# Optimization experiments

Measured on AMD Instinct MI355X. Metric: run time of the kernel, lower is better.

The kernel has to match this reference:

```python
import jax, jax.numpy as jnp
import numpy as np

R = 2                                   # NMS radius (init kwarg r)
EPS = float(np.finfo(np.float32).eps)   # torch.finfo(float32).eps
PI = float(np.pi)


def _sobel(x):
    """Kornia SpatialGradient (sobel, normalized): x [N,1,H,W] -> (dx, dy) each [N,1,H,W]."""
    kx = jnp.array([[-1., 0., 1.], [-2., 0., 2.], [-1., 0., 1.]], jnp.float32) / 8.0
    ky = kx.T
    k = jnp.stack([kx, ky])[:, None]    # [2,1,3,3] -> out channels dx, dy
    xp = jnp.pad(x, ((0, 0), (0, 0), (1, 1), (1, 1)), mode='edge')  # replicate pad
    out = jax.lax.conv_general_dilated(xp, k, (1, 1), 'VALID',
                                       dimension_numbers=('NCHW', 'OIHW', 'NCHW'))
    return out[:, 0:1], out[:, 1:2]


def _theta(mask):
    """Edge direction from one-hot mask, per STEAL edges_nms. mask [N,1,H,W]."""
    dx, dy = _sobel(mask)
    gxx, _ = _sobel(dx)
    gxy, gyy = _sobel(dy)
    return jnp.fmod(jnp.arctan(gyy * jnp.sign(-gxy + EPS) / (gxx + EPS)), PI)


def setup_inputs() -> dict:
    key = jax.random.key(0)
    k1, k2 = jax.random.split(key)
    pred_labels = jax.random.normal(k1, (4, 16, 512, 1024), dtype=jnp.float32)
    true_labels = jax.random.randint(k2, (4, 512, 1024), 0, 16, dtype=jnp.int64)
    return {"pred_labels": pred_labels, "true_labels": true_labels}


def reference(pred_labels, true_labels):
    B, C, H, W = pred_labels.shape
    # per-class one-hot masks -> direction maps
    onehot = jax.nn.one_hot(true_labels, C, dtype=jnp.float32)        # [B,H,W,C]
    masks = onehot.transpose(0, 3, 1, 2).reshape(B * C, 1, H, W)
    theta = _theta(masks).reshape(B, C, H, W)
    thresh_theta = jnp.fmod(jnp.round(theta * (5.0 / PI)) + 5.0, 5.0)  # {0..4}
    dirs = jnp.fmod(thresh_theta, 4.0).astype(jnp.int32)               # {0,1,2,3}

    exp_p = jnp.exp(pred_labels)
    js = list(range(-R, R))
    # offsets (dx_off, dy_off) summed in the denominator for each direction
    offs = {
        0: [(0, j) for j in js],        # horizontal: preds[x, y-r:y+r]
        1: [(j, -j - 1) for j in js],   # anti-diagonal
        2: [(j, 0) for j in js],        # vertical: preds[x-r:x+r, y]
        3: [(-j - 1, j) for j in js],   # anti-diagonal (reversed traversal, same set)
    }
    denom = jnp.ones_like(exp_p)
    for d in range(4):
        dd = exp_p * 0.0
        for ox, oy in offs[d]:
            dd = dd + jnp.roll(exp_p, (-ox, -oy), axis=(2, 3))  # exp_p[x+ox, y+oy]
        denom = jnp.where(dirs == d, dd, denom)

    interior = jnp.zeros((H, W), bool).at[R:H - R, R:W - R].set(True)
    nms = jnp.where(interior, exp_p / denom, 0.0)
    return jnp.sum(nms)
```

## Files before the change

kernel.cpp:

```cpp
#include <hip/hip_runtime.h>


#define Bn 4
#define Cn 16
#define Hn 512
#define Wn 1024

typedef unsigned long long u64;
typedef unsigned int u32;
typedef float f4u __attribute__((ext_vector_type(4), aligned(4)));
typedef int   i4u __attribute__((ext_vector_type(4), aligned(4)));

static __device__ __forceinline__ float fast_rcp(float x) {
#if __has_builtin(__builtin_amdgcn_rcpf)
  return __builtin_amdgcn_rcpf(x);
#else
  return 1.0f / x;
#endif
}


#define P1TW 128
#define P1TH 8
#define P1LW 132
#define P1LH 12

__global__ __launch_bounds__(256)
void dir_kernel(const int* __restrict__ labels, u32* __restrict__ dirs)
{
  __shared__ unsigned char labt[P1LH][P1LW];

  const int w0 = blockIdx.x * P1TW;
  const int h0 = blockIdx.y * P1TH;
  const int b  = blockIdx.z;
  const int tid = threadIdx.x;

  const int* lbase = labels + (size_t)b * (Hn*Wn);
  const bool interior = (h0 >= 2) && (h0 + P1TH + 2 <= Hn) &&
                        (w0 >= 2) && (w0 + P1TW + 2 <= Wn);
  if (interior) {
    const int* lb = lbase + (size_t)(h0-2)*Wn + (w0-2);
    for (int i = tid; i < P1LH*33; i += 256) {
      int row = i / 33, c4 = (i - row*33) * 4;
      i4u L = *(const i4u*)(lb + row*Wn + c4);
      *(u32*)&labt[row][c4] =
          (u32)L.x | ((u32)L.y << 8) | ((u32)L.z << 16) | ((u32)L.w << 24);
    }
  } else {
    for (int i = tid; i < P1LH*33; i += 256) {
      int row = i / 33, c4 = (i - row*33) * 4;
      int gh = min(max(h0-2+row, 0), Hn-1);
      const int* lr = lbase + gh*Wn;
      u32 v = 0;
      #pragma unroll
      for (int k = 0; k < 4; ++k) {
        int gw = min(max(w0-2+c4+k, 0), Wn-1);
        v |= (u32)(lr[gw] & 0xff) << (8*k);
      }
      *(u32*)&labt[row][c4] = v;
    }
  }
  __syncthreads();

  const int tcol = tid & 31;
  const int trow = tid >> 5;

  u64 W[5];
  #pragma unroll
  for (int r = 0; r < 5; ++r) {
    const u32* lp = (const u32*)&labt[trow + r][0];
    u64 lo = lp[tcol];
    u64 hi = lp[tcol + 1];
    W[r] = lo | (hi << 32);
  }

  u32 pack[4] = {0u, 0u, 0u, 0u};

  #pragma unroll 1
  for (int c = 0; c < 16; ++c) {
    const u64 crep = 0x0101010101010101ULL * (u32)c;
    u64 m[5];
    #pragma unroll
    for (int r = 0; r < 5; ++r) {
      u64 x = W[r] ^ crep;
      m[r] = ((0x8080808080808080ULL - x) & 0x8080808080808080ULL) >> 7;
    }
    u64 t  = m[1] + m[3];
    u64 VA = m[0] + m[4] + (t << 2) + (m[2] << 2) + (m[2] << 1);
    u64 VB = ((m[3] << 1) + m[4] + 0x0303030303030303ULL)
             - (m[0] + (m[1] << 1));
    u64 VC = (m[0] + m[4] + 0x0202020202020202ULL) - (m[2] << 1);
    u64 gxxp = (VA + (VA >> 32) + 0x4040404040404040ULL) - ((VA >> 16) << 1);
    u64 q1   = (VC >> 8) + (VC >> 24);
    u64 w16  = VC >> 16;
    u64 gyyp = (VC + (VC >> 32)) + (q1 << 2) + (w16 << 2) + (w16 << 1);
    u64 gxyp = (((VB >> 24) << 1) + (VB >> 32) + 0x2020202020202020ULL)
             - (VB + ((VB >> 8) << 1));

    u32 gxxl = (u32)gxxp, gyyl = (u32)gyyp, gxyl = (u32)gxyp;
    #pragma unroll
    for (int k = 0; k < 4; ++k) {
      int gxx = (int)((gxxl >> (8*k)) & 0xffu) - 64;
      int gyy = (int)((gyyl >> (8*k)) & 0xffu) - 32;
      int gxyb = (int)((gxyl >> (8*k)) & 0xffu);
      int ax = gxx < 0 ? -gxx : gxx;
      int ay = gyy < 0 ? -gyy : gyy;
      int t1 = (__mul24(ay, 100)  > __mul24(ax, 33))   ? 1 : 0;
      int t2 = (__mul24(ay, 1000) > __mul24(ax, 1377)) ? 1 : 0;
      int rb = t1 + t2;
      bool ng = ((gyy < 0) != (gxyb > 32)) != (gxx < 0);
      int dir = ng ? ((rb == 2) ? 3 : 0) : rb;
      pack[k] |= (u32)dir << (2*c);
    }
  }

  const int gh = h0 + trow;
  u32* drow = dirs + ((size_t)b*Hn + gh)*Wn + (w0 + 4*tcol);
  *(uint4*)drow = make_uint4(pack[0], pack[1], pack[2], pack[3]);
}


#define TW 128
#define TH 32
#define LW 132
#define LH 36
#define NT 256

__global__ __launch_bounds__(NT)
void nms_sum_kernel(const float* __restrict__ pred,
                    const u32* __restrict__ dirs,
                    float* __restrict__ slots)
{
  __shared__ float ext[LH*LW];
  __shared__ float wsum[NT/64];

  const int w0 = blockIdx.x * TW;
  const int h0 = blockIdx.y * TH;
  const int bz = blockIdx.z;
  const int b  = bz >> 4;
  const int c  = bz & 15;
  const int tid = threadIdx.x;

  const int x  = tid & 127;
  const int rg = tid >> 7;
  const int gw = w0 + x;

  const u32* dbase = dirs + (size_t)b*Hn*Wn + (size_t)(h0 + rg*16)*Wn + gw;
  u32 dv[16];
  #pragma unroll
  for (int r = 0; r < 16; ++r) dv[r] = dbase[(size_t)r*Wn];

  const float* plane = pred + (size_t)(b*Cn + c) * (size_t)(Hn*Wn);
  const bool interior = (h0 >= 2) && (h0 + TH + 2 <= Hn) &&
                        (w0 >= 2) && (w0 + TW + 2 <= Wn);
  if (interior) {
    const float* pb = plane + (size_t)(h0-2)*Wn + (w0-2);
    for (int i = tid; i < LH*33; i += NT) {
      int row = i / 33, c4 = (i - row*33) * 4;
      f4u p = *(const f4u*)(pb + row*Wn + c4);
      float4 e;
      e.x = __expf(p.x); e.y = __expf(p.y); e.z = __expf(p.z); e.w = __expf(p.w);
      *(float4*)&ext[row*LW + c4] = e;
    }
  } else {
    for (int i = tid; i < LH*(LW/2); i += NT) {
      int row = i / (LW/2);
      int col = (i - row*(LW/2)) * 2;
      int gh = min(max(h0-2+row, 0), Hn-1);
      int ga = min(max(w0-2+col,   0), Wn-1);
      int gb = min(max(w0-1+col,   0), Wn-1);
      const float* prow = plane + gh*Wn;
      *(float2*)&ext[row*LW+col] = make_float2(__expf(prow[ga]), __expf(prow[gb]));
    }
  }
  __syncthreads();

  const bool wv = (gw >= 2) && (gw < Wn-2);
  const u32 sh = 2u * (u32)c;
  const int ghb = h0 + rg*16;

  float acc = 0.f;
  const int abase = (rg*16 + 2)*LW + (x + 2);

  #pragma unroll
  for (int r = 0; r < 16; ++r) {
    const int a0 = abase + r*LW;
    const int dir = (int)((dv[r] >> sh) & 3u);

    const int o0 = (dir == 0) ? -2 : ((dir == 2) ? -264 : -263);
    const int o1 = (dir == 0) ? -1 : -132;
    const int o2 = -(dir & 1);
    const int o3 = (dir == 0) ?  1 : ((dir == 2) ?  132 :  130);

    float g0 = ext[a0 + o0];
    float g1 = ext[a0 + o1];
    float g2 = ext[a0 + o2];
    float g3 = ext[a0 + o3];
    float num = ext[a0];
    float den = ((g0 + g1) + g2) + g3;

    const int gh = ghb + r;
    const bool hv = (gh >= 2) && (gh < Hn-2);
    float nn = (hv && wv) ? num : 0.f;
    acc += nn * fast_rcp(den);
  }

  const int lane = tid & 63;
  const int wq   = tid >> 6;
  #pragma unroll
  for (int off = 32; off > 0; off >>= 1)
    acc += __shfl_down(acc, off);
  if (lane == 0) wsum[wq] = acc;
  __syncthreads();
  if (tid == 0) {
    float s = 0.f;
    #pragma unroll
    for (int q = 0; q < NT/64; ++q) s += wsum[q];
    atomicAdd(&slots[(bz << 2) | (blockIdx.x & 3)], s);
  }
}

__global__ __launch_bounds__(64)
void reduce_ws_kernel(const float* __restrict__ slots, float* __restrict__ out)
{
  const int l = threadIdx.x;
  float s = (slots[l] + slots[l + 64]) + (slots[l + 128] + slots[l + 192]);
  #pragma unroll
  for (int off = 32; off > 0; off >>= 1)
    s += __shfl_down(s, off);
  if (l == 0) *out = s;
}

extern "C" void kernel_launch(void* const* d_in, const int* in_sizes, int n_in,
                              void* d_out, int out_size, void* d_ws, size_t ws_size,
                              hipStream_t stream) {
  (void)in_sizes; (void)n_in; (void)ws_size; (void)out_size;
  const float* pred   = (const float*)d_in[0];
  const int*   labels = (const int*)d_in[1];
  float* out = (float*)d_out;

  u32*   dirs  = (u32*)d_ws;
  float* slots = (float*)((char*)d_ws + (size_t)Bn*Hn*Wn*sizeof(u32));

  hipMemsetAsync(slots, 0, 256 * sizeof(float), stream);

  dir_kernel<<<dim3(Wn/P1TW, Hn/P1TH, Bn), 256, 0, stream>>>(labels, dirs);
  nms_sum_kernel<<<dim3(Wn/TW, Hn/TH, Bn*Cn), NT, 0, stream>>>(pred, dirs, slots);
  reduce_ws_kernel<<<1, 64, 0, stream>>>(slots, out);
}
```

Before: 250.4 us.

## Compute 4x4 pixel tiles per thread with register-resident LDS window reuse

Each thread now handles a 4x4 block of pixels instead of a 1x16 column. It loads the direction words as uint4 vectors and pulls vectorized 8-wide LDS row segments into a rotating register window, so the neighbour taps are selected from registers rather than re-read from LDS per pixel. This is meant to cut LDS traffic and per-pixel address computation, at the cost of more registers and select instructions.

```diff
diff --git a/kernel.cpp b/kernel.cpp
--- a/kernel.cpp
+++ b/kernel.cpp
@@ -141,14 +141,18 @@
   const int c  = bz & 15;
   const int tid = threadIdx.x;
 
-  const int x  = tid & 127;
-  const int rg = tid >> 7;
-  const int gw = w0 + x;
-
-  const u32* dbase = dirs + (size_t)b*Hn*Wn + (size_t)(h0 + rg*16)*Wn + gw;
-  u32 dv[16];
-  #pragma unroll
-  for (int r = 0; r < 16; ++r) dv[r] = dbase[(size_t)r*Wn];
+  const int tc  = tid & 31;
+  const int rg  = tid >> 5;
+  const int x0  = 4*tc;
+  const int r0  = 4*rg;
+  const int gw0 = w0 + x0;
+  const int gh0 = h0 + r0;
+
+  const u32* dbase = dirs + (size_t)b*Hn*Wn + (size_t)gh0*Wn + gw0;
+  const uint4 dq0 = *(const uint4*)(dbase);
+  const uint4 dq1 = *(const uint4*)(dbase + Wn);
+  const uint4 dq2 = *(const uint4*)(dbase + 2*(size_t)Wn);
+  const uint4 dq3 = *(const uint4*)(dbase + 3*(size_t)Wn);
 
   const float* plane = pred + (size_t)(b*Cn + c) * (size_t)(Hn*Wn);
   const bool interior = (h0 >= 2) && (h0 + TH + 2 <= Hn) &&
@@ -175,35 +179,53 @@
   }
   __syncthreads();
 
-  const bool wv = (gw >= 2) && (gw < Wn-2);
   const u32 sh = 2u * (u32)c;
-  const int ghb = h0 + rg*16;
+
+  float p0[8], p1[8], p2[8], p3[8];
+
+#define LDROW(P, TR) { const int _a = ((TR)+2)*LW + x0;                       \
+    const f4u _lo = *(const f4u*)&ext[_a];                                    \
+    const f4u _hi = *(const f4u*)&ext[_a + 4];                                \
+    P[0]=_lo.x; P[1]=_lo.y; P[2]=_lo.z; P[3]=_lo.w;                           \
+    P[4]=_hi.x; P[5]=_hi.y; P[6]=_hi.z; P[7]=_hi.w; }
 
   float acc = 0.f;
-  const int abase = (rg*16 + 2)*LW + (x + 2);
-
-  #pragma unroll
-  for (int r = 0; r < 16; ++r) {
-    const int a0 = abase + r*LW;
-    const int dir = (int)((dv[r] >> sh) & 3u);
-
-    const int o0 = (dir == 0) ? -2 : ((dir == 2) ? -264 : -263);
-    const int o1 = (dir == 0) ? -1 : -132;
-    const int o2 = -(dir & 1);
-    const int o3 = (dir == 0) ?  1 : ((dir == 2) ?  132 :  130);
-
-    float g0 = ext[a0 + o0];
-    float g1 = ext[a0 + o1];
-    float g2 = ext[a0 + o2];
-    float g3 = ext[a0 + o3];
-    float num = ext[a0];
-    float den = ((g0 + g1) + g2) + g3;
-
-    const int gh = ghb + r;
-    const bool hv = (gh >= 2) && (gh < Hn-2);
-    float nn = (hv && wv) ? num : 0.f;
-    acc += nn * fast_rcp(den);
-  }
+
+#define PIX(A,B,Cc,D, I, DW, HV) {                                            \
+    const int d = (int)(((DW) >> sh) & 3u);                                   \
+    const float num = Cc[(I)+2];                                              \
+    const float g0 = (d==0) ? Cc[(I)]   : ((d==2) ? A[(I)+2] : A[(I)+3]);     \
+    const float g1 = (d==0) ? Cc[(I)+1] : B[(I)+2];                           \
+    const float g2 = (d & 1) ? Cc[(I)+1] : num;                               \
+    const float g3 = (d==0) ? Cc[(I)+3] : ((d==2) ? D[(I)+2] : D[(I)]);       \
+    const float den = ((g0 + g1) + g2) + g3;                                  \
+    const bool wvI = (gw0+(I) >= 2) && (gw0+(I) < Wn-2);                      \
+    const float nn = ((HV) && wvI) ? num : 0.f;                               \
+    acc += nn * fast_rcp(den); }
+
+#define ROW(A,B,Cc,D, DQ, S) {                                                \
+    const int gh = gh0 + (S);                                                 \
+    const bool hv = (gh >= 2) && (gh < Hn-2);                                 \
+    PIX(A,B,Cc,D, 0, (DQ).x, hv)                                              \
+    PIX(A,B,Cc,D, 1, (DQ).y, hv)                                              \
+    PIX(A,B,Cc,D, 2, (DQ).z, hv)                                              \
+    PIX(A,B,Cc,D, 3, (DQ).w, hv) }
+
+  LDROW(p0, r0-2)
+  LDROW(p1, r0-1)
+  LDROW(p2, r0+0)
+  LDROW(p3, r0+1)
+  ROW(p0,p1,p2,p3, dq0, 0)
+  LDROW(p0, r0+2)
+  ROW(p1,p2,p3,p0, dq1, 1)
+  LDROW(p1, r0+3)
+  ROW(p2,p3,p0,p1, dq2, 2)
+  LDROW(p2, r0+4)
+  ROW(p3,p0,p1,p2, dq3, 3)
+
+#undef ROW
+#undef PIX
+#undef LDROW
 
   const int lane = tid & 63;
   const int wq   = tid >> 6;
```

New measurement: 247.9 us. About the same (-1.0%).
